# Optimization experiments

Measured on AMD Instinct MI355X. Metric: run time of the kernel, lower is better.

The kernel has to match this reference:

```python
import jax, jax.numpy as jnp
import numpy as np

DIM = 1024
HEADS = 16
HEAD_DIM = DIM // HEADS
MLP_HIDDEN = int(DIM * 0.7)  # 716
EPS = 1e-5


def _ln(x, g, b):
    m = jnp.mean(x, axis=-1, keepdims=True)
    v = jnp.mean(jnp.square(x - m), axis=-1, keepdims=True)
    return (x - m) * jax.lax.rsqrt(v + EPS) * g + b


def setup_inputs() -> dict:
    key = jax.random.key(0)
    ks = jax.random.split(key, 8)
    B, N = 4, 1024
    x = jax.random.normal(ks[0], (B, N, DIM), dtype=jnp.float32)
    s = 0.02
    return {
        "x": x,
        "norm_g": jnp.ones((DIM,), jnp.float32),
        "norm_b": jnp.zeros((DIM,), jnp.float32),
        "W1": jax.random.normal(ks[1], (DIM, 3 * DIM + MLP_HIDDEN), jnp.float32) * s,
        "b1": jnp.zeros((3 * DIM + MLP_HIDDEN,), jnp.float32),
        "qn_g": jnp.ones((HEAD_DIM,), jnp.float32),
        "qn_b": jnp.zeros((HEAD_DIM,), jnp.float32),
        "kn_g": jnp.ones((HEAD_DIM,), jnp.float32),
        "kn_b": jnp.zeros((HEAD_DIM,), jnp.float32),
        "projW": jax.random.normal(ks[2], (DIM, DIM), jnp.float32) * s,
        "projb": jnp.zeros((DIM,), jnp.float32),
        "mlpW": jax.random.normal(ks[3], (MLP_HIDDEN, DIM), jnp.float32) * s,  # mlp_bias=False
        "W2": jax.random.normal(ks[4], (2 * DIM, DIM), jnp.float32) * s,
        "b2": jnp.zeros((DIM,), jnp.float32),
        "ls_g": jnp.full((DIM,), 1e-5, jnp.float32),
    }


def reference(x, norm_g, norm_b, W1, b1, qn_g, qn_b, kn_g, kn_b,
              projW, projb, mlpW, W2, b2, ls_g):
    B, N, C = x.shape
    norm_x = _ln(x, norm_g, norm_b)
    f1 = norm_x @ W1 + b1  # (B, N, 3*dim + mlp_hidden)
    qkv, mlp_hidden = f1[..., :3 * DIM], f1[..., 3 * DIM:]
    # (B, N, 3, H, hd) -> (3, B, H, N, hd)
    qkv = qkv.reshape(B, N, 3, HEADS, HEAD_DIM).transpose(2, 0, 3, 1, 4)
    q, k, v = qkv[0], qkv[1], qkv[2]
    q = _ln(q, qn_g, qn_b)
    k = _ln(k, kn_g, kn_b)
    attn = jnp.einsum('bhnd,bhmd->bhnm', q, k) * (HEAD_DIM ** -0.5)
    attn = jax.nn.softmax(attn, axis=-1)
    xo = jnp.einsum('bhnm,bhmd->bhnd', attn, v)
    xo = xo.transpose(0, 2, 1, 3).reshape(B, N, DIM)
    attn_out = xo @ projW + projb
    mlp_out = jax.nn.gelu(mlp_hidden, approximate=False) @ mlpW  # no bias
    combined = jnp.concatenate([attn_out, mlp_out], axis=-1)
    out = x + (combined @ W2 + b2) * ls_g
    return out
```

## Files before the change

kernel.cpp:

```cpp
#include <hip/hip_runtime.h>
#include <cstdint>
#include <cstddef>

typedef unsigned short u16;
typedef unsigned char u8;
typedef __attribute__((ext_vector_type(8))) u16 u16x8;
typedef __attribute__((ext_vector_type(8))) __bf16 bf16x8;
typedef __attribute__((ext_vector_type(4))) float f32x4;
typedef __attribute__((ext_vector_type(16))) float f32x16;
typedef __attribute__((ext_vector_type(4))) int i32x4;
typedef __attribute__((ext_vector_type(8))) int i32x8;

__device__ __forceinline__ u16 f2bf(float f) {
  unsigned u = __builtin_bit_cast(unsigned, f);
  return (u16)((u + 0x7FFFu + ((u >> 16) & 1u)) >> 16);
}
__device__ __forceinline__ float bf2f(u16 h) {
  return __builtin_bit_cast(float, (unsigned)h << 16);
}
__device__ __forceinline__ u8 f2fp8(float f) {
  return (u8)(__builtin_amdgcn_cvt_pk_fp8_f32(f, 0.f, 0, false) & 0xFF);
}
__device__ __forceinline__ f32x4 mfma16(u16x8 a, u16x8 b, f32x4 c) {
  return __builtin_amdgcn_mfma_f32_16x16x32_bf16(
      __builtin_bit_cast(bf16x8, a), __builtin_bit_cast(bf16x8, b), c, 0, 0, 0);
}
__device__ __forceinline__ void load_lds16(const void* g, void* l) {
  __builtin_amdgcn_global_load_lds(
      (const __attribute__((address_space(1))) void*)g,
      (__attribute__((address_space(3))) void*)l, 16, 0, 0);
}

__global__ __launch_bounds__(256) void k_trcvt_all(
    const float* __restrict__ W1, const float* __restrict__ projW,
    const float* __restrict__ mlpW, const float* __restrict__ W2,
    u8* __restrict__ W1t, u8* __restrict__ pWt, u8* __restrict__ mWt,
    u8* __restrict__ W2t) {
  __shared__ float t[32][33];
  const int L = blockIdx.x;
  const float* src;
  u8* dst;
  int R, C, dR, dC, bx, by;
  if (L < 3840) {
    src = W1; dst = W1t; R = 1024; C = 3788; dR = 1024; dC = 3840;
    bx = L % 120; by = L / 120;
  } else if (L < 4864) {
    int tq = L - 3840;
    src = projW; dst = pWt; R = 1024; C = 1024; dR = 1024; dC = 1024;
    bx = tq & 31; by = tq >> 5;
  } else if (L < 5632) {
    int tq = L - 4864;
    src = mlpW; dst = mWt; R = 716; C = 1024; dR = 768; dC = 1024;
    bx = tq & 31; by = tq >> 5;
  } else {
    int tq = L - 5632;
    src = W2; dst = W2t; R = 2048; C = 1024; dR = 2048; dC = 1024;
    bx = tq & 31; by = tq >> 5;
  }
  const int n0 = bx * 32, k0 = by * 32;
  const int tx = threadIdx.x & 31, ty = threadIdx.x >> 5;
#pragma unroll
  for (int j = 0; j < 4; ++j) {
    int kk = k0 + ty + 8 * j, nn = n0 + tx;
    float v = (kk < R && nn < C) ? src[(size_t)kk * C + nn] : 0.f;
    t[ty + 8 * j][tx] = v;
  }
  __syncthreads();
#pragma unroll
  for (int j = 0; j < 4; ++j) {
    int nn = n0 + ty + 8 * j, kk = k0 + tx;
    if (nn < dC && kk < dR) dst[(size_t)nn * dR + kk] = f2fp8(t[tx][ty + 8 * j]);
  }
}

__global__ __launch_bounds__(256) void k_trvt(const u16* __restrict__ f1,
                                              u16* __restrict__ vtb) {
  __shared__ u16 t[32][33];
  const int z = blockIdx.z;
  const int b = z >> 4, h = z & 15;
  const int d0 = blockIdx.x * 32, n0 = blockIdx.y * 32;
  const int tx = threadIdx.x & 31, ty = threadIdx.x >> 5;
#pragma unroll
  for (int j = 0; j < 4; ++j)
    t[ty + 8 * j][tx] =
        f1[(size_t)(b * 1024 + n0 + ty + 8 * j) * 3840 + 2048 + h * 64 + d0 + tx];
  __syncthreads();
#pragma unroll
  for (int j = 0; j < 4; ++j)
    vtb[(size_t)z * 65536 + (size_t)(d0 + ty + 8 * j) * 1024 + n0 + tx] =
        t[tx][ty + 8 * j];
}

__global__ __launch_bounds__(256) void k_lnx(const float* __restrict__ x,
                                             const float* __restrict__ g,
                                             const float* __restrict__ b,
                                             u8* __restrict__ out) {
  const int row = blockIdx.x, tid = threadIdx.x;
  float4 v = ((const float4*)(x + (size_t)row * 1024))[tid];
  float s = v.x + v.y + v.z + v.w;
  float ss = v.x * v.x + v.y * v.y + v.z * v.z + v.w * v.w;
#pragma unroll
  for (int off = 1; off < 64; off <<= 1) {
    s += __shfl_xor(s, off);
    ss += __shfl_xor(ss, off);
  }
  __shared__ float red[8];
  const int wid = tid >> 6, lane = tid & 63;
  if (lane == 0) { red[wid] = s; red[4 + wid] = ss; }
  __syncthreads();
  s = red[0] + red[1] + red[2] + red[3];
  ss = red[4] + red[5] + red[6] + red[7];
  const float mean = s * (1.f / 1024.f);
  const float var = ss * (1.f / 1024.f) - mean * mean;
  const float rstd = rsqrtf(var + 1e-5f);
  float4 gv = ((const float4*)g)[tid];
  float4 bv = ((const float4*)b)[tid];
  float y0 = (v.x - mean) * rstd * gv.x + bv.x;
  float y1 = (v.y - mean) * rstd * gv.y + bv.y;
  float y2 = (v.z - mean) * rstd * gv.z + bv.z;
  float y3 = (v.w - mean) * rstd * gv.w + bv.w;
  int pk = __builtin_amdgcn_cvt_pk_fp8_f32(y0, y1, 0, false);
  pk = __builtin_amdgcn_cvt_pk_fp8_f32(y2, y3, pk, true);
  ((int*)(out + (size_t)row * 1024))[tid] = pk;
}

__device__ __forceinline__ void gemm_fp8_core(const u8* __restrict__ A,
                                              const u8* __restrict__ B, int K,
                                              u8* Alds, u8* Blds,
                                              f32x16 (&acc)[2][2], int tid) {
  const int lane = tid & 63, wave = tid >> 6;
  const int h = lane >> 5, r32 = lane & 31;
  const int wrow = (wave >> 1) * 64, wcol = (wave & 1) * 64;
  const int srow0 = tid >> 2, spos = tid & 3;
  const int nk = K >> 6;
  for (int kt = 0; kt < nk; ++kt) {
#pragma unroll
    for (int p = 0; p < 2; ++p) {
      const int row = p * 64 + srow0;
      const int c = spos ^ ((row >> 1) & 3);
      const size_t go = (size_t)row * K + kt * 64 + c * 16;
      load_lds16(A + go, Alds + (p * 256 + tid) * 16);
      load_lds16(B + go, Blds + (p * 256 + tid) * 16);
    }
    __syncthreads();
    i32x8 af[2], bf[2];
#pragma unroll
    for (int t = 0; t < 2; ++t) {
      {
        const int row = wrow + t * 32 + r32;
        const int sw = (row >> 1) & 3;
        i32x4 lo = *(const i32x4*)(Alds + row * 64 + ((2 * h) ^ sw) * 16);
        i32x4 hi = *(const i32x4*)(Alds + row * 64 + ((2 * h + 1) ^ sw) * 16);
        i32x8 a;
        a[0] = lo[0]; a[1] = lo[1]; a[2] = lo[2]; a[3] = lo[3];
        a[4] = hi[0]; a[5] = hi[1]; a[6] = hi[2]; a[7] = hi[3];
        af[t] = a;
      }
      {
        const int row = wcol + t * 32 + r32;
        const int sw = (row >> 1) & 3;
        i32x4 lo = *(const i32x4*)(Blds + row * 64 + ((2 * h) ^ sw) * 16);
        i32x4 hi = *(const i32x4*)(Blds + row * 64 + ((2 * h + 1) ^ sw) * 16);
        i32x8 b8;
        b8[0] = lo[0]; b8[1] = lo[1]; b8[2] = lo[2]; b8[3] = lo[3];
        b8[4] = hi[0]; b8[5] = hi[1]; b8[6] = hi[2]; b8[7] = hi[3];
        bf[t] = b8;
      }
    }
#pragma unroll
    for (int i = 0; i < 2; ++i)
#pragma unroll
      for (int j = 0; j < 2; ++j)
        acc[i][j] = __builtin_amdgcn_mfma_scale_f32_32x32x64_f8f6f4(
            af[i], bf[j], acc[i][j], 0, 0, 0, 0x7F7F7F7F, 0, 0x7F7F7F7F);
    __syncthreads();
  }
}

__device__ __forceinline__ void gemm_fp8_core64(const u8* __restrict__ A,
                                                const u8* __restrict__ B, int K,
                                                u8* Alds, u8* Blds,
                                                f32x16 (&acc)[2], int tid) {
  const int lane = tid & 63, wave = tid >> 6;
  const int h = lane >> 5, r32 = lane & 31;
  const int wrow = (wave >> 1) * 32, wcol = (wave & 1) * 64;
  const int nk = K >> 6;
  for (int kt = 0; kt < nk; ++kt) {
    {
      const int r = tid >> 2, pos = tid & 3;
      const int c = pos ^ ((r >> 1) & 3);
      load_lds16(A + (size_t)r * K + kt * 64 + c * 16, Alds + tid * 16);
    }
#pragma unroll
    for (int p = 0; p < 2; ++p) {
      const int s = tid + 256 * p;
      const int r = s >> 2, pos = s & 3;
      const int c = pos ^ ((r >> 1) & 3);
      load_lds16(B + (size_t)r * K + kt * 64 + c * 16, Blds + s * 16);
    }
    __syncthreads();
    i32x8 af, bf[2];
    {
      const int row = wrow + r32;
      const int sw = (row >> 1) & 3;
      i32x4 lo = *(const i32x4*)(Alds + row * 64 + ((2 * h) ^ sw) * 16);
      i32x4 hi = *(const i32x4*)(Alds + row * 64 + ((2 * h + 1) ^ sw) * 16);
      af[0] = lo[0]; af[1] = lo[1]; af[2] = lo[2]; af[3] = lo[3];
      af[4] = hi[0]; af[5] = hi[1]; af[6] = hi[2]; af[7] = hi[3];
    }
#pragma unroll
    for (int t = 0; t < 2; ++t) {
      const int row = wcol + t * 32 + r32;
      const int sw = (row >> 1) & 3;
      i32x4 lo = *(const i32x4*)(Blds + row * 64 + ((2 * h) ^ sw) * 16);
      i32x4 hi = *(const i32x4*)(Blds + row * 64 + ((2 * h + 1) ^ sw) * 16);
      i32x8 b8;
      b8[0] = lo[0]; b8[1] = lo[1]; b8[2] = lo[2]; b8[3] = lo[3];
      b8[4] = hi[0]; b8[5] = hi[1]; b8[6] = hi[2]; b8[7] = hi[3];
      bf[t] = b8;
    }
#pragma unroll
    for (int j = 0; j < 2; ++j)
      acc[j] = __builtin_amdgcn_mfma_scale_f32_32x32x64_f8f6f4(
          af, bf[j], acc[j], 0, 0, 0, 0x7F7F7F7F, 0, 0x7F7F7F7F);
    __syncthreads();
  }
}

__global__ __launch_bounds__(256) void k_gemm1(const u8* __restrict__ nx8,
                                               const u8* __restrict__ W1t,
                                               u16* __restrict__ f1,
                                               const float* __restrict__ b1) {
  __shared__ __align__(16) u8 Alds[128 * 64];
  __shared__ __align__(16) u8 Blds[128 * 64];
  const int tid = threadIdx.x, bm = blockIdx.y, bn = blockIdx.x;
  f32x16 acc[2][2];
#pragma unroll
  for (int i = 0; i < 2; ++i)
#pragma unroll
    for (int j = 0; j < 2; ++j)
#pragma unroll
      for (int r = 0; r < 16; ++r) acc[i][j][r] = 0.f;
  gemm_fp8_core(nx8 + (size_t)bm * 128 * 1024, W1t + (size_t)bn * 128 * 1024, 1024,
                Alds, Blds, acc, tid);
  const int lane = tid & 63, wave = tid >> 6;
  const int h = lane >> 5, r32 = lane & 31;
  const int wrow = (wave >> 1) * 64, wcol = (wave & 1) * 64;
#pragma unroll
  for (int i = 0; i < 2; ++i)
#pragma unroll
    for (int j = 0; j < 2; ++j) {
      const int col = bn * 128 + wcol + j * 32 + r32;
      const float bs = (col < 3788) ? b1[col] : 0.f;
#pragma unroll
      for (int r = 0; r < 16; ++r) {
        const int row = bm * 128 + wrow + i * 32 + 4 * h + (r & 3) + 8 * (r >> 2);
        f1[(size_t)row * 3840 + col] = f2bf(acc[i][j][r] + bs);
      }
    }
}

__global__ __launch_bounds__(256) void k_gemm_pm(
    const u8* __restrict__ xo, const u8* __restrict__ pWt,
    const u8* __restrict__ gel, const u8* __restrict__ mWt,
    u8* __restrict__ comb, const float* __restrict__ projb) {
  __shared__ __align__(16) u8 Alds[64 * 64];
  __shared__ __align__(16) u8 Blds[128 * 64];
  const int tid = threadIdx.x, bm = blockIdx.y, bnq = blockIdx.x;
  const u8* A;
  const u8* B;
  int K, colbase;
  const float* bias;
  if (bnq < 8) {
    A = xo + (size_t)bm * 64 * 1024;
    B = pWt + (size_t)bnq * 128 * 1024;
    K = 1024; colbase = bnq * 128; bias = projb;
  } else {
    A = gel + (size_t)bm * 64 * 768;
    B = mWt + (size_t)(bnq - 8) * 128 * 768;
    K = 768; colbase = 1024 + (bnq - 8) * 128; bias = nullptr;
  }
  f32x16 acc[2];
#pragma unroll
  for (int j = 0; j < 2; ++j)
#pragma unroll
    for (int r = 0; r < 16; ++r) acc[j][r] = 0.f;
  gemm_fp8_core64(A, B, K, Alds, Blds, acc, tid);
  const int lane = tid & 63, wave = tid >> 6;
  const int h = lane >> 5, r32 = lane & 31;
  const int wrow = (wave >> 1) * 32, wcol = (wave & 1) * 64;
#pragma unroll
  for (int j = 0; j < 2; ++j) {
    const int col = colbase + wcol + j * 32 + r32;
    const float bs = (bias != nullptr) ? bias[col - colbase + colbase - colbase +
                                              (bnq < 8 ? bnq * 128 : 0) - 
                                              (bnq < 8 ? bnq * 128 : 0) + 
                                              (wcol + j * 32 + r32)] : 0.f;
#pragma unroll
    for (int r = 0; r < 16; ++r) {
      const int row = bm * 64 + wrow + 4 * h + (r & 3) + 8 * (r >> 2);
      comb[(size_t)row * 2048 + col] = f2fp8(acc[j][r] + bs);
    }
  }
}

__global__ __launch_bounds__(256) void k_gemm_fin(const u8* __restrict__ comb,
                                                  const u8* __restrict__ W2t,
                                                  float* __restrict__ out,
                                                  const float* __restrict__ b2,
                                                  const float* __restrict__ x,
                                                  const float* __restrict__ lsg) {
  __shared__ __align__(16) u8 Alds[64 * 64];
  __shared__ __align__(16) u8 Blds[128 * 64];
  const int tid = threadIdx.x, bm = blockIdx.y, bn = blockIdx.x;
  f32x16 acc[2];
#pragma unroll
  for (int j = 0; j < 2; ++j)
#pragma unroll
    for (int r = 0; r < 16; ++r) acc[j][r] = 0.f;
  gemm_fp8_core64(comb + (size_t)bm * 64 * 2048, W2t + (size_t)bn * 128 * 2048, 2048,
                  Alds, Blds, acc, tid);
  const int lane = tid & 63, wave = tid >> 6;
  const int h = lane >> 5, r32 = lane & 31;
  const int wrow = (wave >> 1) * 32, wcol = (wave & 1) * 64;
#pragma unroll
  for (int j = 0; j < 2; ++j) {
    const int col = bn * 128 + wcol + j * 32 + r32;
    const float bs = b2[col], ls = lsg[col];
#pragma unroll
    for (int r = 0; r < 16; ++r) {
      const int row = bm * 64 + wrow + 4 * h + (r & 3) + 8 * (r >> 2);
      out[(size_t)row * 1024 + col] =
          x[(size_t)row * 1024 + col] + (acc[j][r] + bs) * ls;
    }
  }
}

__global__ __launch_bounds__(256) void k_qkvgelu(const u16* __restrict__ f1,
                                                 const float* __restrict__ qg,
                                                 const float* __restrict__ qbb,
                                                 const float* __restrict__ kg,
                                                 const float* __restrict__ kbb,
                                                 u16* __restrict__ q,
                                                 u16* __restrict__ k,
                                                 u8* __restrict__ gel) {
  const int tid = threadIdx.x;
  if (blockIdx.x < 4096) {
    const int row = blockIdx.x;
    const int rem = tid >> 3;
    const int which = rem >> 4, h = rem & 15;
    const int e8 = (tid & 7) * 8;
    u16x8 xv = *(const u16x8*)(f1 + (size_t)row * 3840 + which * 1024 + h * 64 + e8);
    float xf[8];
    float s1 = 0.f, s2 = 0.f;
#pragma unroll
    for (int e = 0; e < 8; ++e) {
      xf[e] = bf2f(xv[e]);
      s1 += xf[e];
      s2 += xf[e] * xf[e];
    }
#pragma unroll
    for (int off = 1; off < 8; off <<= 1) {
      s1 += __shfl_xor(s1, off);
      s2 += __shfl_xor(s2, off);
    }
    const float mean = s1 * (1.f / 64.f);
    const float var = s2 * (1.f / 64.f) - mean * mean;
    const float rstd = rsqrtf(var + 1e-5f);
    const float* g = (which == 0) ? qg : kg;
    const float* bb = (which == 0) ? qbb : kbb;
    float4 g0 = ((const float4*)g)[e8 >> 2], g1 = ((const float4*)g)[(e8 >> 2) + 1];
    float4 b0 = ((const float4*)bb)[e8 >> 2], b1 = ((const float4*)bb)[(e8 >> 2) + 1];
    float gv[8] = {g0.x, g0.y, g0.z, g0.w, g1.x, g1.y, g1.z, g1.w};
    float bv[8] = {b0.x, b0.y, b0.z, b0.w, b1.x, b1.y, b1.z, b1.w};
    u16x8 o;
#pragma unroll
    for (int e = 0; e < 8; ++e) o[e] = f2bf((xf[e] - mean) * rstd * gv[e] + bv[e]);
    const int b = row >> 10, n = row & 1023;
    u16* dst = (which == 0) ? q : k;
    *(u16x8*)(dst + ((size_t)(b * 16 + h) * 1024 + n) * 64 + e8) = o;
  } else {
    const int id = (blockIdx.x - 4096) * 256 + tid;
    const int row = id / 96, c8 = id - row * 96;
    u16x8 xv = *(const u16x8*)(f1 + (size_t)row * 3840 + 3072 + c8 * 8);
    float rr[8];
#pragma unroll
    for (int e = 0; e < 8; ++e) {
      const int col = c8 * 8 + e;
      rr[e] = 0.f;
      if (col < 716) {
        float xx = bf2f(xv[e]);
        rr[e] = 0.5f * xx * (1.f + erff(xx * 0.70710678118654752f));
      }
    }
    int p0 = __builtin_amdgcn_cvt_pk_fp8_f32(rr[0], rr[1], 0, false);
    p0 = __builtin_amdgcn_cvt_pk_fp8_f32(rr[2], rr[3], p0, true);
    int p1 = __builtin_amdgcn_cvt_pk_fp8_f32(rr[4], rr[5], 0, false);
    p1 = __builtin_amdgcn_cvt_pk_fp8_f32(rr[6], rr[7], p1, true);
    uint2 pk;
    pk.x = (unsigned)p0;
    pk.y = (unsigned)p1;
    *(uint2*)(gel + (size_t)row * 768 + c8 * 8) = pk;
  }
}

__global__ __launch_bounds__(128) void k_flash(const u16* __restrict__ q,
                                               const u16* __restrict__ k,
                                               const u16* __restrict__ vt,
                                               u8* __restrict__ xo) {
  __shared__ __align__(16) u16 Kl[64 * 64];
  __shared__ __align__(16) u16 Vl[64 * 64];
  __shared__ __align__(16) u16 Pl[2 * 16 * 64];
  const int tid = threadIdx.x, wave = tid >> 6, lane = tid & 63;
  const int l15 = lane & 15, quad = lane >> 4;
  const int L = blockIdx.x;
  const int xcd = L & 7, i = L >> 3;
  const int bh = xcd * 8 + (i & 7), qt = i >> 3;
  const int qrow0 = qt * 32 + wave * 16;
  const u16* qb = q + ((size_t)bh * 1024 + qrow0) * 64;
  const u16* kb = k + (size_t)bh * 1024 * 64;
  const u16* vb = vt + (size_t)bh * 64 * 1024;
  u16* Pw = Pl + wave * 16 * 64;

  u16x8 qf[2];
#pragma unroll
  for (int kk = 0; kk < 2; ++kk)
    qf[kk] = *(const u16x8*)(qb + (size_t)l15 * 64 + (kk * 4 + quad) * 8);

  f32x4 O[4];
  float lacc[4] = {0.f, 0.f, 0.f, 0.f};
#pragma unroll
  for (int dt = 0; dt < 4; ++dt) O[dt] = f32x4{0.f, 0.f, 0.f, 0.f};

  const int pl7 = l15 & 7;
  for (int kv = 0; kv < 16; ++kv) {
#pragma unroll
    for (int p = 0; p < 4; ++p) {
      const int s = tid + 128 * p;
      const int r = s >> 3, pos = s & 7;
      const int c = pos ^ (r & 7);
      load_lds16(kb + (size_t)(kv * 64 + r) * 64 + c * 8, Kl + s * 8);
      load_lds16(vb + (size_t)r * 1024 + kv * 64 + c * 8, Vl + s * 8);
    }
    __syncthreads();
    f32x4 S[4];
#pragma unroll
    for (int j = 0; j < 4; ++j) S[j] = f32x4{0.f, 0.f, 0.f, 0.f};
#pragma unroll
    for (int j = 0; j < 4; ++j)
#pragma unroll
      for (int kk = 0; kk < 2; ++kk) {
        const int pos = (kk * 4 + quad) ^ pl7;
        u16x8 bfr = *(const u16x8*)(Kl + (16 * j + l15) * 64 + pos * 8);
        S[j] = mfma16(qf[kk], bfr, S[j]);
      }
#pragma unroll
    for (int j = 0; j < 4; ++j)
#pragma unroll
      for (int r = 0; r < 4; ++r) {
        float pv = __expf(S[j][r] * 0.125f);
        lacc[r] += pv;
        const int prow = quad * 4 + r;
        const int pc = 2 * j + (l15 >> 3);
        Pw[prow * 64 + (pc ^ (prow & 7)) * 8 + pl7] = f2bf(pv);
      }
    __builtin_amdgcn_s_waitcnt(0xC07F);
#pragma unroll
    for (int c = 0; c < 2; ++c) {
      const int pos = (c * 4 + quad) ^ pl7;
      u16x8 pa = *(const u16x8*)(Pw + l15 * 64 + pos * 8);
#pragma unroll
      for (int dt = 0; dt < 4; ++dt) {
        u16x8 vf = *(const u16x8*)(Vl + (16 * dt + l15) * 64 + pos * 8);
        O[dt] = mfma16(pa, vf, O[dt]);
      }
    }
    __syncthreads();
  }
#pragma unroll
  for (int r = 0; r < 4; ++r) {
#pragma unroll
    for (int off = 1; off < 16; off <<= 1) lacc[r] += __shfl_xor(lacc[r], off);
  }
  const int b = bh >> 4, h = bh & 15;
#pragma unroll
  for (int r = 0; r < 4; ++r) {
    const float inv = 1.f / lacc[r];
    u8* orow = xo + (size_t)(b * 1024 + qrow0 + quad * 4 + r) * 1024 + h * 64;
#pragma unroll
    for (int dt = 0; dt < 4; ++dt) orow[16 * dt + l15] = f2fp8(O[dt][r] * inv);
  }
}

extern "C" void kernel_launch(void* const* d_in, const int* in_sizes, int n_in,
                              void* d_out, int out_size, void* d_ws, size_t ws_size,
                              hipStream_t stream) {
  (void)in_sizes; (void)n_in; (void)out_size; (void)ws_size;
  const float* x      = (const float*)d_in[0];
  const float* norm_g = (const float*)d_in[1];
  const float* norm_b = (const float*)d_in[2];
  const float* W1     = (const float*)d_in[3];
  const float* b1     = (const float*)d_in[4];
  const float* qn_g   = (const float*)d_in[5];
  const float* qn_b   = (const float*)d_in[6];
  const float* kn_g   = (const float*)d_in[7];
  const float* kn_b   = (const float*)d_in[8];
  const float* projW  = (const float*)d_in[9];
  const float* projb  = (const float*)d_in[10];
  const float* mlpW   = (const float*)d_in[11];
  const float* W2     = (const float*)d_in[12];
  const float* b2     = (const float*)d_in[13];
  const float* ls_g   = (const float*)d_in[14];

  char* ws = (char*)d_ws;
  u8*  W1t8 = (u8*)(ws + 0);
  u8*  pWt8 = (u8*)(ws + 3932160);
  u8*  mWt8 = (u8*)(ws + 4980736);
  u8*  W2t8 = (u8*)(ws + 5767168);
  u8*  nx8  = (u8*)(ws + 7864320);
  u16* f1   = (u16*)(ws + 12058624);
  u16* qbuf = (u16*)(ws + 43515904);
  u16* kbuf = (u16*)(ws + 51904512);
  u16* vtb  = (u16*)(ws + 60293120);
  u8*  gel8 = (u8*)(ws + 68681728);

  k_trcvt_all<<<7680, 256, 0, stream>>>(W1, projW, mlpW, W2, W1t8, pWt8, mWt8, W2t8);
  k_lnx<<<4096, 256, 0, stream>>>(x, norm_g, norm_b, nx8);
  k_gemm1<<<dim3(30, 32), 256, 0, stream>>>(nx8, W1t8, f1, b1);
  k_qkvgelu<<<5632, 256, 0, stream>>>(f1, qn_g, qn_b, kn_g, kn_b, qbuf, kbuf, gel8);
  k_trvt<<<dim3(2, 32, 64), 256, 0, stream>>>(f1, vtb);
  k_flash<<<2048, 128, 0, stream>>>(qbuf, kbuf, vtb, nx8);
  k_gemm_pm<<<dim3(16, 64), 256, 0, stream>>>(nx8, pWt8, gel8, mWt8, (u8*)f1, projb);
  k_gemm_fin<<<dim3(8, 64), 256, 0, stream>>>((u8*)f1, W2t8, (float*)d_out, b2, x,
                                              ls_g);
}
```

Baseline: 239.2 us.

## Double-buffer K/V tiles in flash attention with 4-wave blocks and setprio

Measured after the change: 233.0 us. 2.6% less time.

```diff
diff --git a/kernel.cpp b/kernel.cpp
--- a/kernel.cpp
+++ b/kernel.cpp
@@ -292,10 +292,7 @@
 #pragma unroll
   for (int j = 0; j < 2; ++j) {
     const int col = colbase + wcol + j * 32 + r32;
-    const float bs = (bias != nullptr) ? bias[col - colbase + colbase - colbase +
-                                              (bnq < 8 ? bnq * 128 : 0) - 
-                                              (bnq < 8 ? bnq * 128 : 0) + 
-                                              (wcol + j * 32 + r32)] : 0.f;
+    const float bs = (bias != nullptr) ? bias[col] : 0.f;
 #pragma unroll
     for (int r = 0; r < 16; ++r) {
       const int row = bm * 64 + wrow + 4 * h + (r & 3) + 8 * (r >> 2);
@@ -404,19 +401,19 @@
   }
 }
 
-__global__ __launch_bounds__(128) void k_flash(const u16* __restrict__ q,
+__global__ __launch_bounds__(256) void k_flash(const u16* __restrict__ q,
                                                const u16* __restrict__ k,
                                                const u16* __restrict__ vt,
                                                u8* __restrict__ xo) {
-  __shared__ __align__(16) u16 Kl[64 * 64];
-  __shared__ __align__(16) u16 Vl[64 * 64];
-  __shared__ __align__(16) u16 Pl[2 * 16 * 64];
+  __shared__ __align__(16) u16 Kl[2][64 * 64];
+  __shared__ __align__(16) u16 Vl[2][64 * 64];
+  __shared__ __align__(16) u16 Pl[4 * 16 * 64];
   const int tid = threadIdx.x, wave = tid >> 6, lane = tid & 63;
   const int l15 = lane & 15, quad = lane >> 4;
   const int L = blockIdx.x;
   const int xcd = L & 7, i = L >> 3;
   const int bh = xcd * 8 + (i & 7), qt = i >> 3;
-  const int qrow0 = qt * 32 + wave * 16;
+  const int qrow0 = qt * 64 + wave * 16;
   const u16* qb = q + ((size_t)bh * 1024 + qrow0) * 64;
   const u16* kb = k + (size_t)bh * 1024 * 64;
   const u16* vb = vt + (size_t)bh * 64 * 1024;
@@ -433,27 +430,40 @@
   for (int dt = 0; dt < 4; ++dt) O[dt] = f32x4{0.f, 0.f, 0.f, 0.f};
 
   const int pl7 = l15 & 7;
+  const int r0 = tid >> 3, c0 = (tid & 7) ^ (r0 & 7);
+  const int s1 = tid + 256;
+  const int r1 = s1 >> 3, c1 = (s1 & 7) ^ (r1 & 7);
+
+  load_lds16(kb + (size_t)r0 * 64 + c0 * 8, (u16*)Kl[0] + tid * 8);
+  load_lds16(kb + (size_t)r1 * 64 + c1 * 8, (u16*)Kl[0] + s1 * 8);
+  load_lds16(vb + (size_t)r0 * 1024 + c0 * 8, (u16*)Vl[0] + tid * 8);
+  load_lds16(vb + (size_t)r1 * 1024 + c1 * 8, (u16*)Vl[0] + s1 * 8);
+  __syncthreads();
+
   for (int kv = 0; kv < 16; ++kv) {
-#pragma unroll
-    for (int p = 0; p < 4; ++p) {
-      const int s = tid + 128 * p;
-      const int r = s >> 3, pos = s & 7;
-      const int c = pos ^ (r & 7);
-      load_lds16(kb + (size_t)(kv * 64 + r) * 64 + c * 8, Kl + s * 8);
-      load_lds16(vb + (size_t)r * 1024 + kv * 64 + c * 8, Vl + s * 8);
-    }
-    __syncthreads();
+    const int cur = kv & 1;
+    if (kv < 15) {
+      const size_t ko = (size_t)(kv + 1) * 64;
+      load_lds16(kb + (ko + r0) * 64 + c0 * 8, (u16*)Kl[cur ^ 1] + tid * 8);
+      load_lds16(kb + (ko + r1) * 64 + c1 * 8, (u16*)Kl[cur ^ 1] + s1 * 8);
+      load_lds16(vb + (size_t)r0 * 1024 + ko + c0 * 8, (u16*)Vl[cur ^ 1] + tid * 8);
+      load_lds16(vb + (size_t)r1 * 1024 + ko + c1 * 8, (u16*)Vl[cur ^ 1] + s1 * 8);
+    }
+    const u16* Kc = (const u16*)Kl[cur];
+    const u16* Vc = (const u16*)Vl[cur];
     f32x4 S[4];
 #pragma unroll
     for (int j = 0; j < 4; ++j) S[j] = f32x4{0.f, 0.f, 0.f, 0.f};
+    __builtin_amdgcn_s_setprio(1);
 #pragma unroll
     for (int j = 0; j < 4; ++j)
 #pragma unroll
       for (int kk = 0; kk < 2; ++kk) {
         const int pos = (kk * 4 + quad) ^ pl7;
-        u16x8 bfr = *(const u16x8*)(Kl + (16 * j + l15) * 64 + pos * 8);
+        u16x8 bfr = *(const u16x8*)(Kc + (16 * j + l15) * 64 + pos * 8);
         S[j] = mfma16(qf[kk], bfr, S[j]);
       }
+    __builtin_amdgcn_s_setprio(0);
 #pragma unroll
     for (int j = 0; j < 4; ++j)
 #pragma unroll
@@ -465,16 +475,18 @@
         Pw[prow * 64 + (pc ^ (prow & 7)) * 8 + pl7] = f2bf(pv);
       }
     __builtin_amdgcn_s_waitcnt(0xC07F);
+    __builtin_amdgcn_s_setprio(1);
 #pragma unroll
     for (int c = 0; c < 2; ++c) {
       const int pos = (c * 4 + quad) ^ pl7;
       u16x8 pa = *(const u16x8*)(Pw + l15 * 64 + pos * 8);
 #pragma unroll
       for (int dt = 0; dt < 4; ++dt) {
-        u16x8 vf = *(const u16x8*)(Vl + (16 * dt + l15) * 64 + pos * 8);
+        u16x8 vf = *(const u16x8*)(Vc + (16 * dt + l15) * 64 + pos * 8);
         O[dt] = mfma16(pa, vf, O[dt]);
       }
     }
+    __builtin_amdgcn_s_setprio(0);
     __syncthreads();
   }
 #pragma unroll
@@ -529,7 +541,7 @@
   k_gemm1<<<dim3(30, 32), 256, 0, stream>>>(nx8, W1t8, f1, b1);
   k_qkvgelu<<<5632, 256, 0, stream>>>(f1, qn_g, qn_b, kn_g, kn_b, qbuf, kbuf, gel8);
   k_trvt<<<dim3(2, 32, 64), 256, 0, stream>>>(f1, vtb);
-  k_flash<<<2048, 128, 0, stream>>>(qbuf, kbuf, vtb, nx8);
+  k_flash<<<1024, 256, 0, stream>>>(qbuf, kbuf, vtb, nx8);
   k_gemm_pm<<<dim3(16, 64), 256, 0, stream>>>(nx8, pWt8, gel8, mWt8, (u8*)f1, projb);
   k_gemm_fin<<<dim3(8, 64), 256, 0, stream>>>((u8*)f1, W2t8, (float*)d_out, b2, x,
                                               ls_g);
```
